# Kernel optimization log

Hardware: AMD Instinct MI355X
Metric: run time of the kernel (lower is better)

Reference implementation:

```python
import jax, jax.numpy as jnp
import numpy as np

HIDDEN = 512

def setup_inputs() -> dict:
    key = jax.random.key(0)
    ks = jax.random.split(key, 11)
    B, T, I, H, O = 256, 512, 2, HIDDEN, 11
    s = lambda k, shp, sc=0.05: jax.random.normal(k, shp, dtype=jnp.float32) * sc
    return {
        "inputs": jax.random.normal(ks[0], (B, T, I), dtype=jnp.float32),
        "w_ih1": s(ks[1], (I, 4 * H)),
        "w_hh1": s(ks[2], (H, 4 * H)),
        "b_ih1": s(ks[3], (4 * H,)),
        "b_hh1": s(ks[4], (4 * H,)),
        "w_ih2": s(ks[5], (H, 4 * H)),
        "w_hh2": s(ks[6], (H, 4 * H)),
        "b_ih2": s(ks[7], (4 * H,)),
        "b_hh2": s(ks[8], (4 * H,)),
        "fc_w": s(ks[9], (H, O)),
        "fc_b": s(ks[10], (O,)),
    }

def _lstm_step(x, h, c, w_ih, w_hh, b):
    # x: [B, D_in], h/c: [B, H]; gate order (i, f, g, o) as in tf.split
    gates = x @ w_ih + h @ w_hh + b  # [B, 4H]
    i, f, g, o = jnp.split(gates, 4, axis=1)
    c_new = jax.nn.sigmoid(f) * c + jax.nn.sigmoid(i) * jnp.tanh(g)
    h_new = jax.nn.sigmoid(o) * jnp.tanh(c_new)
    return h_new, c_new

def reference(inputs, w_ih1, w_hh1, b_ih1, b_hh1, w_ih2, w_hh2, b_ih2, b_hh2, fc_w, fc_b):
    B = inputs.shape[0]
    H = HIDDEN
    b1 = b_ih1 + b_hh1  # fold the two biases (mathematically identical)
    b2 = b_ih2 + b_hh2
    # Precompute input projections for layer 1 across all timesteps (one big GEMM).
    x_proj = jnp.einsum('bti,ih->bth', inputs, w_ih1) + b1  # [B, T, 4H]

    def step(carry, xp_t):
        h1, c1, h2, c2 = carry
        gates1 = xp_t + h1 @ w_hh1
        i1, f1, g1, o1 = jnp.split(gates1, 4, axis=1)
        c1 = jax.nn.sigmoid(f1) * c1 + jax.nn.sigmoid(i1) * jnp.tanh(g1)
        h1 = jax.nn.sigmoid(o1) * jnp.tanh(c1)
        h2, c2 = _lstm_step(h1, h2, c2, w_ih2, w_hh2, b2)
        return (h1, c1, h2, c2), None

    z = jnp.zeros((B, H), dtype=inputs.dtype)
    (h1, c1, h2, c2), _ = jax.lax.scan(step, (z, z, z, z), jnp.swapaxes(x_proj, 0, 1))
    logits = h2 @ fc_w + fc_b
    return jax.nn.softmax(logits, axis=-1)
```

## Files before the change

### kernel.cpp

```cpp
#include <hip/hip_runtime.h>
#include <hip/hip_bf16.h>

#define Tz  512
#define Hz  512
#define BHz (256*512)
#define NBLK 192
#define HB4 (BHz/4)

typedef __bf16 bf16x8 __attribute__((ext_vector_type(8)));
typedef float  f32x4  __attribute__((ext_vector_type(4)));
typedef unsigned u32x4 __attribute__((ext_vector_type(4)));
typedef unsigned long long ull;

#define MFMA16(A,B,C) __builtin_amdgcn_mfma_f32_16x16x32_bf16(A,B,C,0,0,0)

__device__ __forceinline__ float sigf(float x){ return 1.0f/(1.0f+__expf(-x)); }
__device__ __forceinline__ float tanhf_(float x){ return 2.0f/(1.0f+__expf(-2.0f*x)) - 1.0f; }

__device__ __forceinline__ unsigned cload32(const unsigned* p){
    return __hip_atomic_load(p, __ATOMIC_RELAXED, __HIP_MEMORY_SCOPE_AGENT);
}
__device__ __forceinline__ void cstore32(unsigned* p, unsigned v){
    __hip_atomic_store(p, v, __ATOMIC_RELAXED, __HIP_MEMORY_SCOPE_AGENT);
}

__global__ void pack_w1(const float* __restrict__ w, __bf16* __restrict__ out){
    int idx = blockIdx.x*256 + threadIdx.x;
    int i = idx & 7, lane = (idx>>3)&63, kb = (idx>>9)&15, jt = idx>>13;
    int k  = kb*32 + (lane>>4)*8 + i;
    int m  = lane & 15;
    int col = (m&3)*512 + jt*4 + (m>>2);
    out[idx] = (__bf16)w[k*2048 + col];
}
__global__ void pack_w2(const float* __restrict__ wih, const float* __restrict__ whh,
                        __bf16* __restrict__ out){
    int idx = blockIdx.x*256 + threadIdx.x;
    int i = idx & 7, lane = (idx>>3)&63, kb = (idx>>9)&31, jt = idx>>14;
    int k  = kb*32 + (lane>>4)*8 + i;
    int m  = lane & 15;
    int col = (m&3)*512 + jt*4 + (m>>2);
    float val = (k < 512) ? wih[k*2048 + col] : whh[(k-512)*2048 + col];
    out[idx] = (__bf16)val;
}
__global__ void pack_bias(const float* a, const float* b, const float* c, const float* d,
                          float* b1s, float* b2s){
    int i = blockIdx.x*256 + threadIdx.x;
    if (i < 2048){ b1s[i] = a[i]+b[i]; b2s[i] = c[i]+d[i]; }
}

__device__ __forceinline__ void issue8(u32x4* r, const ull* src, int tid){
    #pragma unroll
    for (int i = 0; i < 8; ++i){
        int c = tid + 256*i;
        const ull* p = src + (size_t)(c>>6)*128 + (size_t)(c&63)*2;
        asm volatile("global_load_dwordx4 %0, %1, off sc0 sc1" : "=v"(r[i]) : "v"(p) : "memory");
    }
}
__device__ __forceinline__ void write8(bf16x8* sh, const u32x4* r, int tid){
    #pragma unroll
    for (int i = 0; i < 8; ++i){
        int c = tid + 256*i;
        union { u32x4 u; bf16x8 v; } U; U.u = r[i];
        sh[c ^ ((c>>6) & 7)] = U.v;
    }
}
#define DRAIN() do { asm volatile("s_waitcnt vmcnt(0)" ::: "memory"); \
                     __builtin_amdgcn_sched_barrier(0); } while(0)

__device__ __forceinline__ void cstore128(ull* p, ull lo, ull hi){
    union { ull q2[2]; u32x4 u; } S; S.q2[0] = lo; S.q2[1] = hi;
    asm volatile("global_store_dwordx4 %0, %1, off sc0 sc1" :: "v"(p), "v"(S.u) : "memory");
}

__device__ __forceinline__ void pollL1(const unsigned* fbase, int tid, unsigned tgt){
    if (tid < 8){ const unsigned* fp = fbase + tid*16;
        while (cload32(fp) < tgt) {} }
    __builtin_amdgcn_s_barrier();
}
__device__ __forceinline__ void pollL2(const unsigned* fbase, int tid, unsigned tgt){
    if (tid < 16){ const unsigned* fp = fbase + (8+tid)*16;
        while (cload32(fp) < tgt) {} }
    __builtin_amdgcn_s_barrier();
}

__launch_bounds__(256, 1)
__global__ void lstm_persistent(const float* __restrict__ x,
                                const float* __restrict__ wih1,
                                const float* __restrict__ b1s,
                                const float* __restrict__ b2s,
                                const __bf16* __restrict__ w1p,
                                const __bf16* __restrict__ w2p,
                                __bf16* __restrict__ h1b,
                                __bf16* __restrict__ h2b,
                                unsigned* __restrict__ flags)
{
    __shared__ bf16x8 sh[4096];
    const int bid = blockIdx.x;
    const int g   = bid & 7;
    const int t   = bid >> 3;
    unsigned* fbase = flags + g*384;

    const int tid  = threadIdx.x;
    const int v    = tid >> 6;
    const int lane = tid & 63;
    const int llo  = lane & 15, lhi = lane >> 4;
    const int sw   = llo & 7;

    const ull* h1u = (const ull*)h1b;
    const ull* h2u = (const ull*)h2b;
    const size_t bandoff = (size_t)g*32*128;

    if (t < 8){
        const int jt0 = t*16 + v*4;
        bf16x8 wf[4][16];
        #pragma unroll
        for (int m = 0; m < 4; ++m)
            #pragma unroll
            for (int kb = 0; kb < 16; ++kb)
                wf[m][kb] = *reinterpret_cast<const bf16x8*>(
                    w1p + ((size_t)((jt0+m)*16 + kb)*64 + lane)*8);
        float wa[4][4], wb[4][4], bb[4][4];
        #pragma unroll
        for (int m = 0; m < 4; ++m)
            #pragma unroll
            for (int q = 0; q < 4; ++q){
                int col = q*512 + (jt0+m)*4 + lhi;
                wa[m][q] = wih1[col]; wb[m][q] = wih1[2048 + col]; bb[m][q] = b1s[col];
            }
        const float2* x2 = reinterpret_cast<const float2*>(x);
        float c1[4][2] = {{0,0},{0,0},{0,0},{0,0}};

        for (int p = 0; p < Tz; ++p){
            pollL1(fbase, tid, (unsigned)p);
            u32x4 rA[8];
            issue8(rA, h1u + (size_t)((p+3)&3)*HB4 + bandoff, tid);
            DRAIN();
            write8(sh, rA, tid);
            __syncthreads();
            f32x4 acc[4][2];
            #pragma unroll
            for (int m = 0; m < 4; ++m){ acc[m][0] = (f32x4){0,0,0,0}; acc[m][1] = (f32x4){0,0,0,0}; }
            #pragma unroll
            for (int nt = 0; nt < 2; ++nt){
                const int base = (nt*16 + llo) << 6;
                #pragma unroll
                for (int kb = 0; kb < 16; ++kb){
                    bf16x8 bf = sh[(base + kb*4 + lhi) ^ sw];
                    acc[0][nt] = MFMA16(wf[0][kb], bf, acc[0][nt]);
                    acc[1][nt] = MFMA16(wf[1][kb], bf, acc[1][nt]);
                    acc[2][nt] = MFMA16(wf[2][kb], bf, acc[2][nt]);
                    acc[3][nt] = MFMA16(wf[3][kb], bf, acc[3][nt]);
                }
            }
            ull pkk[2][4];
            #pragma unroll
            for (int nt = 0; nt < 2; ++nt){
                int row = g*32 + nt*16 + llo;
                float2 xv = x2[(size_t)row*Tz + p];
                #pragma unroll
                for (int m = 0; m < 4; ++m){
                    float gi = acc[m][nt][0] + xv.x*wa[m][0] + xv.y*wb[m][0] + bb[m][0];
                    float gf = acc[m][nt][1] + xv.x*wa[m][1] + xv.y*wb[m][1] + bb[m][1];
                    float gg = acc[m][nt][2] + xv.x*wa[m][2] + xv.y*wb[m][2] + bb[m][2];
                    float go = acc[m][nt][3] + xv.x*wa[m][3] + xv.y*wb[m][3] + bb[m][3];
                    float cn = sigf(gf)*c1[m][nt] + sigf(gi)*tanhf_(gg);
                    c1[m][nt] = cn;
                    __bf16 hv = (__bf16)(sigf(go)*tanhf_(cn));
                    unsigned hb_;
                    { union { __bf16 b; unsigned short s; } C; C.b = hv; hb_ = C.s; }
                    unsigned s1 = __shfl(hb_, llo+16, 64);
                    unsigned s2 = __shfl(hb_, llo+32, 64);
                    unsigned s3 = __shfl(hb_, llo+48, 64);
                    pkk[nt][m] = (ull)hb_ | ((ull)s1<<16) | ((ull)s2<<32) | ((ull)s3<<48);
                }
            }
            pollL2(fbase, tid, (p >= 3) ? (unsigned)(p-3) : 0u);
            ull* h1n = (ull*)h1b + (size_t)(p&3)*HB4;
            if (lane < 16){
                #pragma unroll
                for (int nt = 0; nt < 2; ++nt){
                    int row = g*32 + nt*16 + llo;
                    ull* dst = h1n + (size_t)row*128 + jt0;
                    cstore128(dst,     pkk[nt][0], pkk[nt][1]);
                    cstore128(dst + 2, pkk[nt][2], pkk[nt][3]);
                }
            }
            __syncthreads();
            if (tid == 0) cstore32(fbase + t*16, (unsigned)(p+1));
        }
    } else {
        const int u   = t - 8;
        const int jt0 = u*8 + v*2;
        bf16x8 wf[2][32];
        #pragma unroll
        for (int m = 0; m < 2; ++m)
            #pragma unroll
            for (int kb = 0; kb < 32; ++kb)
                wf[m][kb] = *reinterpret_cast<const bf16x8*>(
                    w2p + ((size_t)((jt0+m)*32 + kb)*64 + lane)*8);
        float bb2[2][4];
        #pragma unroll
        for (int m = 0; m < 2; ++m)
            #pragma unroll
            for (int q = 0; q < 4; ++q)
                bb2[m][q] = b2s[q*512 + (jt0+m)*4 + lhi];
        float c2[2][2] = {{0,0},{0,0}};

        for (int q = 1; q <= Tz; ++q){
            pollL2(fbase, tid, (unsigned)(q-1));
            u32x4 rB[8];
            issue8(rB, h2u + (size_t)((q+2)&3)*HB4 + bandoff, tid);
            pollL1(fbase, tid, (unsigned)q);
            u32x4 rA[8];
            issue8(rA, h1u + (size_t)((q+3)&3)*HB4 + bandoff, tid);
            DRAIN();
            write8(sh,        rA, tid);
            write8(sh + 2048, rB, tid);
            __syncthreads();
            f32x4 acc[2][2];
            acc[0][0]=(f32x4){0,0,0,0}; acc[0][1]=(f32x4){0,0,0,0};
            acc[1][0]=(f32x4){0,0,0,0}; acc[1][1]=(f32x4){0,0,0,0};
            #pragma unroll
            for (int nt = 0; nt < 2; ++nt){
                const int base = (nt*16 + llo) << 6;
                #pragma unroll
                for (int kb = 0; kb < 16; ++kb){
                    bf16x8 bf = sh[(base + kb*4 + lhi) ^ sw];
                    acc[0][nt] = MFMA16(wf[0][kb], bf, acc[0][nt]);
                    acc[1][nt] = MFMA16(wf[1][kb], bf, acc[1][nt]);
                }
                #pragma unroll
                for (int kb = 16; kb < 32; ++kb){
                    bf16x8 bf = sh[2048 + ((base + (kb-16)*4 + lhi) ^ sw)];
                    acc[0][nt] = MFMA16(wf[0][kb], bf, acc[0][nt]);
                    acc[1][nt] = MFMA16(wf[1][kb], bf, acc[1][nt]);
                }
            }
            ull* h2n = (ull*)h2b + (size_t)((q+3)&3)*HB4;
            #pragma unroll
            for (int nt = 0; nt < 2; ++nt){
                int row = g*32 + nt*16 + llo;
                ull pk[2];
                #pragma unroll
                for (int m = 0; m < 2; ++m){
                    float gi = acc[m][nt][0] + bb2[m][0];
                    float gf = acc[m][nt][1] + bb2[m][1];
                    float gg = acc[m][nt][2] + bb2[m][2];
                    float go = acc[m][nt][3] + bb2[m][3];
                    float cn = sigf(gf)*c2[m][nt] + sigf(gi)*tanhf_(gg);
                    c2[m][nt] = cn;
                    __bf16 hv = (__bf16)(sigf(go)*tanhf_(cn));
                    unsigned hb_;
                    { union { __bf16 b; unsigned short s; } C; C.b = hv; hb_ = C.s; }
                    unsigned s1 = __shfl(hb_, llo+16, 64);
                    unsigned s2 = __shfl(hb_, llo+32, 64);
                    unsigned s3 = __shfl(hb_, llo+48, 64);
                    pk[m] = (ull)hb_ | ((ull)s1<<16) | ((ull)s2<<32) | ((ull)s3<<48);
                }
                if (lane < 16){
                    ull* dst = h2n + (size_t)row*128 + jt0;
                    cstore128(dst, pk[0], pk[1]);
                }
            }
            __syncthreads();
            if (tid == 0) cstore32(fbase + t*16, (unsigned)q);
        }
    }
}

__global__ void logits_softmax(const __bf16* __restrict__ h2, const float* __restrict__ fcw,
                               const float* __restrict__ fcb, float* __restrict__ out)
{
    int row = blockIdx.x;
    int lane = threadIdx.x;
    float acc[11];
    #pragma unroll
    for (int o = 0; o < 11; ++o) acc[o] = 0.f;
    for (int it = 0; it < 8; ++it){
        int jj = it*64 + lane;
        float hv = (float)h2[row*512 + jj];
        #pragma unroll
        for (int o = 0; o < 11; ++o) acc[o] += hv * fcw[jj*11 + o];
    }
    #pragma unroll
    for (int o = 0; o < 11; ++o)
        for (int s = 32; s >= 1; s >>= 1) acc[o] += __shfl_xor(acc[o], s, 64);
    float m = -1e30f;
    #pragma unroll
    for (int o = 0; o < 11; ++o){ acc[o] += fcb[o]; m = fmaxf(m, acc[o]); }
    float ssum = 0.f;
    #pragma unroll
    for (int o = 0; o < 11; ++o){ acc[o] = __expf(acc[o] - m); ssum += acc[o]; }
    float inv = 1.0f/ssum;
    if (lane < 11) out[row*11 + lane] = acc[lane]*inv;
}

extern "C" void kernel_launch(void* const* d_in, const int* in_sizes, int n_in,
                              void* d_out, int out_size, void* d_ws, size_t ws_size,
                              hipStream_t stream)
{
    const float* x    = (const float*)d_in[0];
    const float* wih1 = (const float*)d_in[1];
    const float* whh1 = (const float*)d_in[2];
    const float* bih1 = (const float*)d_in[3];
    const float* bhh1 = (const float*)d_in[4];
    const float* wih2 = (const float*)d_in[5];
    const float* whh2 = (const float*)d_in[6];
    const float* bih2 = (const float*)d_in[7];
    const float* bhh2 = (const float*)d_in[8];
    const float* fcw  = (const float*)d_in[9];
    const float* fcb  = (const float*)d_in[10];
    float* out = (float*)d_out;

    char* p = (char*)d_ws;
    __bf16* w1p = (__bf16*)p;  p += (size_t)512*2048*2;
    __bf16* w2p = (__bf16*)p;  p += (size_t)1024*2048*2;
    float*  b1s = (float*)p;   p += 2048*4;
    float*  b2s = (float*)p;   p += 2048*4;
    __bf16* h1b = (__bf16*)p;  p += (size_t)4*BHz*2;
    __bf16* h2b = (__bf16*)p;  p += (size_t)4*BHz*2;
    unsigned* flags = (unsigned*)p; p += 8*384*4;

    (void)hipMemsetAsync(h1b, 0, (size_t)4*BHz*2, stream);
    (void)hipMemsetAsync(h2b, 0, (size_t)4*BHz*2, stream);
    (void)hipMemsetAsync(flags, 0, 8*384*4, stream);
    pack_w1 <<<4096, 256, 0, stream>>>(whh1, w1p);
    pack_w2 <<<8192, 256, 0, stream>>>(wih2, whh2, w2p);
    pack_bias<<<8,   256, 0, stream>>>(bih1, bhh1, bih2, bhh2, b1s, b2s);

    lstm_persistent<<<NBLK, 256, 0, stream>>>(x, wih1, b1s, b2s, w1p, w2p, h1b, h2b, flags);

    logits_softmax<<<256, 64, 0, stream>>>(h2b + (size_t)3*BHz, fcw, fcb, out);
}
```

Measured before the change: 3.169 ms.

## Replicate hidden-state buffers and flags across four copies to spread reader traffic

```diff
diff --git a/kernel.cpp b/kernel.cpp
--- a/kernel.cpp
+++ b/kernel.cpp
@@ -6,6 +6,7 @@
 #define BHz (256*512)
 #define NBLK 192
 #define HB4 (BHz/4)
+#define REPS 4
 
 typedef __bf16 bf16x8 __attribute__((ext_vector_type(8)));
 typedef float  f32x4  __attribute__((ext_vector_type(4)));
@@ -72,13 +73,13 @@
     asm volatile("global_store_dwordx4 %0, %1, off sc0 sc1" :: "v"(p), "v"(S.u) : "memory");
 }
 
-__device__ __forceinline__ void pollL1(const unsigned* fbase, int tid, unsigned tgt){
-    if (tid < 8){ const unsigned* fp = fbase + tid*16;
+__device__ __forceinline__ void pollL1(const unsigned* fb, int tid, unsigned tgt){
+    if (tid < 8){ const unsigned* fp = fb + tid*16;
         while (cload32(fp) < tgt) {} }
     __builtin_amdgcn_s_barrier();
 }
-__device__ __forceinline__ void pollL2(const unsigned* fbase, int tid, unsigned tgt){
-    if (tid < 16){ const unsigned* fp = fbase + (8+tid)*16;
+__device__ __forceinline__ void pollL2(const unsigned* fb, int tid, unsigned tgt){
+    if (tid < 16){ const unsigned* fp = fb + (8+tid)*16;
         while (cload32(fp) < tgt) {} }
     __builtin_amdgcn_s_barrier();
 }
@@ -98,7 +99,8 @@
     const int bid = blockIdx.x;
     const int g   = bid & 7;
     const int t   = bid >> 3;
-    unsigned* fbase = flags + g*384;
+    const int rep = t & 3;
+    unsigned* fbase = flags + (size_t)(g*REPS + rep)*24*16;
 
     const int tid  = threadIdx.x;
     const int v    = tid >> 6;
@@ -109,6 +111,7 @@
     const ull* h1u = (const ull*)h1b;
     const ull* h2u = (const ull*)h2b;
     const size_t bandoff = (size_t)g*32*128;
+    const size_t repstr  = (size_t)4*HB4;
 
     if (t < 8){
         const int jt0 = t*16 + v*4;
@@ -133,7 +136,7 @@
         for (int p = 0; p < Tz; ++p){
             pollL1(fbase, tid, (unsigned)p);
             u32x4 rA[8];
-            issue8(rA, h1u + (size_t)((p+3)&3)*HB4 + bandoff, tid);
+            issue8(rA, h1u + (size_t)rep*repstr + (size_t)((p+3)&3)*HB4 + bandoff, tid);
             DRAIN();
             write8(sh, rA, tid);
             __syncthreads();
@@ -180,13 +183,21 @@
                 #pragma unroll
                 for (int nt = 0; nt < 2; ++nt){
                     int row = g*32 + nt*16 + llo;
-                    ull* dst = h1n + (size_t)row*128 + jt0;
-                    cstore128(dst,     pkk[nt][0], pkk[nt][1]);
-                    cstore128(dst + 2, pkk[nt][2], pkk[nt][3]);
+                    ull* dst0 = h1n + (size_t)row*128 + jt0;
+                    #pragma unroll
+                    for (int rp = 0; rp < REPS; ++rp){
+                        ull* dst = dst0 + (size_t)rp*repstr;
+                        cstore128(dst,     pkk[nt][0], pkk[nt][1]);
+                        cstore128(dst + 2, pkk[nt][2], pkk[nt][3]);
+                    }
                 }
             }
             __syncthreads();
-            if (tid == 0) cstore32(fbase + t*16, (unsigned)(p+1));
+            if (tid == 0){
+                #pragma unroll
+                for (int rp = 0; rp < REPS; ++rp)
+                    cstore32(flags + (size_t)(g*REPS + rp)*24*16 + t*16, (unsigned)(p+1));
+            }
         }
     } else {
         const int u   = t - 8;
@@ -209,10 +220,10 @@
         for (int q = 1; q <= Tz; ++q){
             pollL2(fbase, tid, (unsigned)(q-1));
             u32x4 rB[8];
-            issue8(rB, h2u + (size_t)((q+2)&3)*HB4 + bandoff, tid);
+            issue8(rB, h2u + (size_t)rep*repstr + (size_t)((q+2)&3)*HB4 + bandoff, tid);
             pollL1(fbase, tid, (unsigned)q);
             u32x4 rA[8];
-            issue8(rA, h1u + (size_t)((q+3)&3)*HB4 + bandoff, tid);
+            issue8(rA, h1u + (size_t)rep*repstr + (size_t)((q+3)&3)*HB4 + bandoff, tid);
             DRAIN();
             write8(sh,        rA, tid);
             write8(sh + 2048, rB, tid);
@@ -258,12 +269,18 @@
                     pk[m] = (ull)hb_ | ((ull)s1<<16) | ((ull)s2<<32) | ((ull)s3<<48);
                 }
                 if (lane < 16){
-                    ull* dst = h2n + (size_t)row*128 + jt0;
-                    cstore128(dst, pk[0], pk[1]);
+                    ull* dst0 = h2n + (size_t)row*128 + jt0;
+                    #pragma unroll
+                    for (int rp = 0; rp < REPS; ++rp)
+                        cstore128(dst0 + (size_t)rp*repstr, pk[0], pk[1]);
                 }
             }
             __syncthreads();
-            if (tid == 0) cstore32(fbase + t*16, (unsigned)q);
+            if (tid == 0){
+                #pragma unroll
+                for (int rp = 0; rp < REPS; ++rp)
+                    cstore32(flags + (size_t)(g*REPS + rp)*24*16 + t*16, (unsigned)q);
+            }
         }
     }
 }
@@ -317,13 +334,13 @@
     __bf16* w2p = (__bf16*)p;  p += (size_t)1024*2048*2;
     float*  b1s = (float*)p;   p += 2048*4;
     float*  b2s = (float*)p;   p += 2048*4;
-    __bf16* h1b = (__bf16*)p;  p += (size_t)4*BHz*2;
-    __bf16* h2b = (__bf16*)p;  p += (size_t)4*BHz*2;
-    unsigned* flags = (unsigned*)p; p += 8*384*4;
-
-    (void)hipMemsetAsync(h1b, 0, (size_t)4*BHz*2, stream);
-    (void)hipMemsetAsync(h2b, 0, (size_t)4*BHz*2, stream);
-    (void)hipMemsetAsync(flags, 0, 8*384*4, stream);
+    __bf16* h1b = (__bf16*)p;  p += (size_t)REPS*4*BHz*2;
+    __bf16* h2b = (__bf16*)p;  p += (size_t)REPS*4*BHz*2;
+    unsigned* flags = (unsigned*)p; p += (size_t)8*REPS*24*16*4;
+
+    (void)hipMemsetAsync(h1b, 0, (size_t)REPS*4*BHz*2, stream);
+    (void)hipMemsetAsync(h2b, 0, (size_t)REPS*4*BHz*2, stream);
+    (void)hipMemsetAsync(flags, 0, (size_t)8*REPS*24*16*4, stream);
     pack_w1 <<<4096, 256, 0, stream>>>(whh1, w1p);
     pack_w2 <<<8192, 256, 0, stream>>>(wih2, whh2, w2p);
     pack_bias<<<8,   256, 0, stream>>>(bih1, bhh1, bih2, bhh2, b1s, b2s);
```

New measurement: 3.972 ms. 25.3% more time.
